# Kernel tuning notes

Hardware: AMD Instinct MI355X
Metric: run time of the kernel (lower is better)

The kernel has to match this reference:

```python
import jax, jax.numpy as jnp
import numpy as np

# ---- quantization scales (per-tensor, as produced by from_float calibration) ----
IN_SCALE = 0.05      # ForwardTokenizer: fp32 hidden -> int8
ALPHA_Q = 1e-4       # W8A8B8O8 requant multipliers (already include 1/sqrt(head_dim) for q)
ALPHA_K = 1e-4
ALPHA_V = 1e-4
QK_ALPHA = 1e-3      # BMM_S8T_S8N_F32T dequant scale (q_scale * k_scale)
PV_ALPHA = 1.0/127.0 # BMM_S8T_S8N_S8T requant scale ((1/127)*v_scale/out_scale)
OUT_ALPHA = 1e-4     # W8A8BFP32OFP32 dequant scale
NUM_HEADS = 32


def _quant_i8(x, scale):
    # simulate int8 quantization in fp32 (values are exact small integers)
    return jnp.clip(jnp.round(x / scale), -128.0, 127.0)


def _w8a8b8o8(x_i8, W_i8, b_i8, alpha):
    # int8 GEMM with int8 bias, requantized to int8: clamp(round(alpha*(x@W^T) + b))
    acc = jnp.einsum('btd,ed->bte', x_i8, W_i8)  # int32 accumulator in fp32
    return jnp.clip(jnp.round(alpha * acc + b_i8), -128.0, 127.0)


def setup_inputs() -> dict:
    key = jax.random.key(0)
    ks = jax.random.split(key, 10)
    B, T, D = 2, 2048, 2560
    hidden_states = jax.random.normal(ks[0], (B, T, D), dtype=jnp.float32)
    # causal additive mask, shape (B,1,T,T)
    neg = jnp.float32(-1e9)
    causal = jnp.where(jnp.tril(jnp.ones((T, T), dtype=bool)), 0.0, neg)
    attention_mask = jnp.broadcast_to(causal[None, None], (B, 1, T, T)).astype(jnp.float32)
    # int8-valued weights/biases stored as fp32 integers in [-127,127]
    def i8(k, shape):
        return jax.random.randint(k, shape, -127, 128).astype(jnp.float32)
    Wq = i8(ks[1], (D, D)); bq = i8(ks[2], (D,))
    Wk = i8(ks[3], (D, D)); bk = i8(ks[4], (D,))
    Wv = i8(ks[5], (D, D)); bv = i8(ks[6], (D,))
    Wo = i8(ks[7], (D, D))
    bo = jax.random.normal(ks[8], (D,), dtype=jnp.float32) * 0.01  # fp32 out bias
    return {"hidden_states": hidden_states, "attention_mask": attention_mask,
            "Wq": Wq, "bq": bq, "Wk": Wk, "bk": bk, "Wv": Wv, "bv": bv,
            "Wo": Wo, "bo": bo}


def reference(hidden_states, attention_mask, Wq, bq, Wk, bk, Wv, bv, Wo, bo):
    B, T, D = hidden_states.shape
    H = NUM_HEADS
    Dh = D // H
    # ForwardTokenizer: fp32 -> int8
    x_i8 = _quant_i8(hidden_states, IN_SCALE)
    # fused int8 q/k/v projections (W8A8B8O8Linear)
    q = _w8a8b8o8(x_i8, Wq, bq, ALPHA_Q)
    k = _w8a8b8o8(x_i8, Wk, bk, ALPHA_K)
    v = _w8a8b8o8(x_i8, Wv, bv, ALPHA_V)
    # (B,T,D) -> (B,H,T,Dh)
    def shape(t):
        return t.reshape(B, T, H, Dh).transpose(0, 2, 1, 3)
    q, k, v = shape(q), shape(k), shape(v)
    # BMM_S8T_S8N_F32T: int8 q @ k^T dequantized to fp32
    attn_weights = QK_ALPHA * jnp.einsum('bhqd,bhkd->bhqk', q, k)
    attn_weights = attn_weights + attention_mask  # (B,H,T,T)
    attn_weights = jnp.maximum(attn_weights, jnp.finfo(jnp.float32).min)
    attn_probs = jax.nn.softmax(attn_weights, axis=-1)
    # requantize probs to int8: mul_(127).round_()
    p_i8 = jnp.round(attn_probs * 127.0)
    # BMM_S8T_S8N_S8T: int8 p @ v requantized to int8
    attn_out = jnp.clip(jnp.round(PV_ALPHA * jnp.einsum('bhqk,bhkd->bhqd', p_i8, v)), -128.0, 127.0)
    # (B,H,T,Dh) -> (B,T,D)
    attn_out = attn_out.transpose(0, 2, 1, 3).reshape(B, T, D)
    # W8A8BFP32OFP32Linear: int8 GEMM, fp32 dequant + fp32 bias
    out = OUT_ALPHA * jnp.einsum('btd,ed->bte', attn_out, Wo) + bo
    return out
```

## Files before the change

kernel.cpp:

```cpp
#include <hip/hip_runtime.h>
#include <stdint.h>

typedef int v4i __attribute__((ext_vector_type(4)));

#define MFMA_I8(a,b,c) __builtin_amdgcn_mfma_i32_16x16x64_i8(a,b,c,0,0,0)

#define TD 2560
#define TT 2048
#define TB 2
#define TH 32
#define TDH 80
#define TDHP 128
#define TM 4096

#define LOG2E_MS 1.4426950408889634e-3f
#define MASKI (-(1<<30))

__device__ __forceinline__ float clamp8f(float v){ return fminf(fmaxf(v, -128.0f), 127.0f); }
__device__ __forceinline__ float fexp2(float x){ return __builtin_amdgcn_exp2f(x); }

__device__ __forceinline__ void gl_lds16(const int8_t* g, int8_t* l){
  __builtin_amdgcn_global_load_lds(
      (const __attribute__((address_space(1))) void*)g,
      (__attribute__((address_space(3))) void*)l, 16, 0, 0);
}

__global__ void k_quant(const float* __restrict__ x, int8_t* __restrict__ y, int n4){
  int stride = gridDim.x * blockDim.x;
  for (int i = blockIdx.x*blockDim.x + threadIdx.x; i < n4; i += stride){
    float4 v = ((const float4*)x)[i];
    char4 o;
    o.x = (int8_t)clamp8f(rintf(__fdiv_rn(v.x, 0.05f)));
    o.y = (int8_t)clamp8f(rintf(__fdiv_rn(v.y, 0.05f)));
    o.z = (int8_t)clamp8f(rintf(__fdiv_rn(v.z, 0.05f)));
    o.w = (int8_t)clamp8f(rintf(__fdiv_rn(v.w, 0.05f)));
    ((char4*)y)[i] = o;
  }
}

__global__ void k_conv(const float* __restrict__ w, int8_t* __restrict__ y, int n4){
  int stride = gridDim.x * blockDim.x;
  for (int i = blockIdx.x*blockDim.x + threadIdx.x; i < n4; i += stride){
    float4 v = ((const float4*)w)[i];
    char4 o;
    o.x = (int8_t)(int)rintf(v.x);
    o.y = (int8_t)(int)rintf(v.y);
    o.z = (int8_t)(int)rintf(v.z);
    o.w = (int8_t)(int)rintf(v.w);
    ((char4*)y)[i] = o;
  }
}

__global__ __launch_bounds__(256, 2) void k_gemm128(const int8_t* __restrict__ x,
    const int8_t* __restrict__ w, const float* __restrict__ bias,
    void* __restrict__ dst, int mode)
{
  __shared__ __align__(16) int8_t As[128*64];
  __shared__ __align__(16) int8_t Bs[128*64];
  const int m0 = blockIdx.x * 128, n0 = blockIdx.y * 128;
  const int t = threadIdx.x;
  const int wv = t >> 6, l = t & 63, lhi = (l >> 4) & 3, llo = l & 15;
  const int wr = wv >> 1, wc = wv & 1;
  const int grow = l >> 2, gcol = (l & 3) * 16;

  const int8_t* xa0 = x + (size_t)(m0 + wv*16 + grow)*TD + gcol;
  const int8_t* xa1 = x + (size_t)(m0 + 64 + wv*16 + grow)*TD + gcol;
  const int8_t* wb0 = w + (size_t)(n0 + wv*16 + grow)*TD + gcol;
  const int8_t* wb1 = w + (size_t)(n0 + 64 + wv*16 + grow)*TD + gcol;
  int8_t* la0 = &As[(wv*16)*64];
  int8_t* la1 = &As[(64 + wv*16)*64];
  int8_t* lb0 = &Bs[(wv*16)*64];
  int8_t* lb1 = &Bs[(64 + wv*16)*64];

  v4i acc[4][4] = {};
  for (int k0 = 0; k0 < TD; k0 += 64){
    gl_lds16(xa0 + k0, la0);
    gl_lds16(xa1 + k0, la1);
    gl_lds16(wb0 + k0, lb0);
    gl_lds16(wb1 + k0, lb1);
    __syncthreads();
    v4i a[4], b[4];
    #pragma unroll
    for (int mi = 0; mi < 4; ++mi)
      a[mi] = *(const v4i*)&As[(wr*64 + mi*16 + llo)*64 + lhi*16];
    #pragma unroll
    for (int ni = 0; ni < 4; ++ni)
      b[ni] = *(const v4i*)&Bs[(wc*64 + ni*16 + llo)*64 + lhi*16];
    #pragma unroll
    for (int mi = 0; mi < 4; ++mi)
      #pragma unroll
      for (int ni = 0; ni < 4; ++ni)
        acc[mi][ni] = MFMA_I8(a[mi], b[ni], acc[mi][ni]);
    __syncthreads();
  }

  #pragma unroll
  for (int mi = 0; mi < 4; ++mi)
  #pragma unroll
  for (int ni = 0; ni < 4; ++ni)
  #pragma unroll
  for (int r = 0; r < 4; ++r){
    int rowg = m0 + wr*64 + mi*16 + lhi*4 + r;
    int colg = n0 + wc*64 + ni*16 + llo;
    float fv = __fadd_rn(__fmul_rn(1e-4f, (float)acc[mi][ni][r]), bias[colg]);
    if (mode == 2){
      ((float*)dst)[(size_t)rowg*TD + colg] = fv;
    } else {
      int8_t q8 = (int8_t)clamp8f(rintf(fv));
      int bb = rowg >> 11, tl = rowg & 2047;
      int hh = colg / 80, dh = colg - hh*80;
      if (mode == 0) ((int8_t*)dst)[((size_t)(bb*TH + hh)*TT + tl)*TDHP + dh] = q8;
      else           ((int8_t*)dst)[((size_t)(bb*TH + hh)*TDH + dh)*TT + tl] = q8;
    }
  }
}

__global__ __launch_bounds__(256, 4) void k_attn5(const int8_t* __restrict__ qb_,
    const int8_t* __restrict__ kb_, const int8_t* __restrict__ vt_,
    int8_t* __restrict__ ao)
{
  __shared__ __align__(16) int8_t Ks[64*128];
  const int flat = blockIdx.x;
  const int g = flat & 7, ii = flat >> 3;
  const int pair = g*8 + (ii >> 4);
  const int j = ii & 15;
  const int h = pair & 31, b = pair >> 5;

  const int t = threadIdx.x, wv = t >> 6, l = t & 63, lhi = (l >> 4) & 3, llo = l & 15;
  const size_t bh = (size_t)(b*TH + h);
  const int8_t* qb = qb_ + bh*TT*TDHP;
  const int8_t* kb = kb_ + bh*TT*TDHP;
  const int8_t* vb = vt_ + bh*TDH*TT;

  const int srow = t >> 2, scp = (t & 3) * 2, ssw = srow & 7;
  const int8_t* kg = kb + (size_t)srow*TDHP + scp*16;
  int8_t* sdst0 = &Ks[srow*128 + (((scp  ) ^ ssw) << 4)];
  int8_t* sdst1 = &Ks[srow*128 + (((scp+1) ^ ssw) << 4)];

  #pragma unroll 1
  for (int half = 0; half < 2; ++half){
    const int qt2 = half ? j : (31 - j);
    const int qw0 = qt2*64 + wv*16;
    const int qg = qw0 + llo;
    const int ktmax = qt2 + 1;

    v4i qa0 = *(const v4i*)(qb + (size_t)(qw0 + llo)*TDHP + lhi*16);
    v4i qa1 = *(const v4i*)(qb + (size_t)(qw0 + llo)*TDHP + 64 + lhi*16);

    int   M  = MASKI;
    float cm = __fmul_rn(LOG2E_MS, (float)MASKI);
    float ls = 0.0f;

    v4i pr0 = *(const v4i*)(kg);
    v4i pr1 = *(const v4i*)(kg + 16);
    *(v4i*)sdst0 = pr0; *(v4i*)sdst1 = pr1;
    for (int kt = 0; kt < ktmax; ++kt){
      if (kt + 1 < ktmax){
        pr0 = *(const v4i*)(kg + (size_t)(kt+1)*64*TDHP);
        pr1 = *(const v4i*)(kg + (size_t)(kt+1)*64*TDHP + 16);
      }
      __syncthreads();
      const int rem = qw0 + 15 - kt*64;
      int sv[4][4];
      #pragma unroll
      for (int sub = 0; sub < 4; ++sub){
        if (sub*16 <= rem){
          const int row = sub*16 + llo, sw = row & 7;
          v4i kf0 = *(const v4i*)&Ks[row*128 + (((lhi  ) ^ sw) << 4)];
          v4i kf1 = *(const v4i*)&Ks[row*128 + (((lhi+4) ^ sw) << 4)];
          v4i d = {}; d = MFMA_I8(kf0, qa0, d); d = MFMA_I8(kf1, qa1, d);
          const int base = kt*64 + sub*16 + lhi*4;
          #pragma unroll
          for (int r = 0; r < 4; ++r)
            sv[sub][r] = (base + r <= qg) ? d[r] : MASKI;
        } else {
          #pragma unroll
          for (int r = 0; r < 4; ++r) sv[sub][r] = MASKI;
        }
      }
      int t0 = max(sv[0][0], sv[0][1]), t1 = max(sv[0][2], sv[0][3]);
      int t2 = max(sv[1][0], sv[1][1]), t3 = max(sv[1][2], sv[1][3]);
      int t4 = max(sv[2][0], sv[2][1]), t5 = max(sv[2][2], sv[2][3]);
      int t6 = max(sv[3][0], sv[3][1]), t7 = max(sv[3][2], sv[3][3]);
      int tm = max(max(max(t0,t1),max(t2,t3)), max(max(t4,t5),max(t6,t7)));
      int Mn = max(M, tm);
      float cmN = __fmul_rn(LOG2E_MS, (float)Mn);
      float fac = fexp2(__fsub_rn(cm, cmN));
      float e[16];
      #pragma unroll
      for (int sub = 0; sub < 4; ++sub)
        #pragma unroll
        for (int r = 0; r < 4; ++r)
          e[sub*4+r] = fexp2(__fmaf_rn((float)sv[sub][r], LOG2E_MS, -cmN));
      float a01 = __fadd_rn(e[0],e[1]),  a23 = __fadd_rn(e[2],e[3]);
      float a45 = __fadd_rn(e[4],e[5]),  a67 = __fadd_rn(e[6],e[7]);
      float a89 = __fadd_rn(e[8],e[9]),  aab = __fadd_rn(e[10],e[11]);
      float acd = __fadd_rn(e[12],e[13]), aef = __fadd_rn(e[14],e[15]);
      float b0 = __fadd_rn(a01,a23), b1 = __fadd_rn(a45,a67);
      float b2 = __fadd_rn(a89,aab), b3 = __fadd_rn(acd,aef);
      float tot = __fadd_rn(__fadd_rn(b0,b1), __fadd_rn(b2,b3));
      ls = __fadd_rn(__fmul_rn(ls, fac), tot);
      M = Mn; cm = cmN;
      __syncthreads();
      if (kt + 1 < ktmax){ *(v4i*)sdst0 = pr0; *(v4i*)sdst1 = pr1; }
    }

    {
      float mm = cm, ll = ls;
      #pragma unroll
      for (int off = 16; off < 64; off <<= 1){
        float om = __shfl_xor(mm, off);
        float ol = __shfl_xor(ll, off);
        float mn = fmaxf(mm, om);
        ll = __fadd_rn(__fmul_rn(ll, fexp2(__fsub_rn(mm, mn))),
                       __fmul_rn(ol, fexp2(__fsub_rn(om, mn))));
        mm = mn;
      }
      cm = mm;
      ls = __fdiv_rn(127.0f, ll);
    }

    v4i pacc[5] = {};
    pr0 = *(const v4i*)(kg);
    pr1 = *(const v4i*)(kg + 16);
    *(v4i*)sdst0 = pr0; *(v4i*)sdst1 = pr1;
    for (int kt = 0; kt < ktmax; ++kt){
      if (kt + 1 < ktmax){
        pr0 = *(const v4i*)(kg + (size_t)(kt+1)*64*TDHP);
        pr1 = *(const v4i*)(kg + (size_t)(kt+1)*64*TDHP + 16);
      }
      __syncthreads();
      const int rem = qw0 + 15 - kt*64;
      uint32_t w[4] = {0u,0u,0u,0u};
      #pragma unroll
      for (int sub = 0; sub < 4; ++sub){
        if (sub*16 <= rem){
          const int row = sub*16 + llo, sw = row & 7;
          v4i kf0 = *(const v4i*)&Ks[row*128 + (((lhi  ) ^ sw) << 4)];
          v4i kf1 = *(const v4i*)&Ks[row*128 + (((lhi+4) ^ sw) << 4)];
          v4i d = {}; d = MFMA_I8(kf0, qa0, d); d = MFMA_I8(kf1, qa1, d);
          const int base = kt*64 + sub*16 + lhi*4;
          uint32_t wrd = 0u;
          #pragma unroll
          for (int r = 0; r < 4; ++r){
            int sel = (base + r <= qg) ? d[r] : MASKI;
            float ev = fexp2(__fmaf_rn((float)sel, LOG2E_MS, -cm));
            int p = (int)rintf(__fmul_rn(ev, ls));
            wrd |= ((uint32_t)(uint8_t)p) << (8*r);
          }
          w[sub] = wrd;
        }
      }
      #pragma unroll
      for (int bb = 0; bb < 2; ++bb){
        const int dist = 16 << bb;
        const int gb = (lhi >> bb) & 1;
        uint32_t nw[4];
        #pragma unroll
        for (int s = 0; s < 4; ++s){
          uint32_t tv = __shfl_xor(w[s ^ (1 << bb)], dist);
          nw[s] = (((s >> bb) & 1) == gb) ? w[s] : tv;
        }
        w[0]=nw[0]; w[1]=nw[1]; w[2]=nw[2]; w[3]=nw[3];
      }
      v4i pa;
      pa[0]=(int)w[0]; pa[1]=(int)w[1]; pa[2]=(int)w[2]; pa[3]=(int)w[3];
      #pragma unroll
      for (int dt = 0; dt < 5; ++dt){
        v4i vf = *(const v4i*)(vb + (size_t)(dt*16 + llo)*TT + kt*64 + lhi*16);
        pacc[dt] = MFMA_I8(vf, pa, pacc[dt]);
      }
      __syncthreads();
      if (kt + 1 < ktmax){ *(v4i*)sdst0 = pr0; *(v4i*)sdst1 = pr1; }
    }

    #pragma unroll
    for (int dt = 0; dt < 5; ++dt){
      uint32_t ob = 0u;
      #pragma unroll
      for (int r = 0; r < 4; ++r){
        int vq = (int)clamp8f(rintf(__fmul_rn((float)pacc[dt][r], (float)(1.0/127.0))));
        ob |= ((uint32_t)(uint8_t)(int8_t)vq) << (8*r);
      }
      *(uint32_t*)(ao + ((size_t)(b*TT) + qw0 + llo)*TD + h*TDH + dt*16 + lhi*4) = ob;
    }
  }
}

extern "C" void kernel_launch(void* const* d_in, const int* in_sizes, int n_in,
                              void* d_out, int out_size, void* d_ws, size_t ws_size,
                              hipStream_t stream) {
  const float* hidden = (const float*)d_in[0];
  const float* Wq = (const float*)d_in[2];
  const float* bq = (const float*)d_in[3];
  const float* Wk = (const float*)d_in[4];
  const float* bk = (const float*)d_in[5];
  const float* Wv = (const float*)d_in[6];
  const float* bv = (const float*)d_in[7];
  const float* Wo = (const float*)d_in[8];
  const float* bo = (const float*)d_in[9];
  float* out = (float*)d_out;

  char* ws = (char*)d_ws;
  const size_t SZ_X  = (size_t)TM * TD;
  const size_t SZ_W  = (size_t)TD * TD;
  const size_t SZ_QK = (size_t)TB * TH * TT * TDHP;
  const size_t SZ_V  = (size_t)TB * TH * TDH * TT;
  int8_t* x8   = (int8_t*)ws;
  int8_t* wq8  = (int8_t*)(ws + SZ_X);
  int8_t* wk8  = wq8 + SZ_W;
  int8_t* wv8  = wk8 + SZ_W;
  int8_t* wo8  = wv8 + SZ_W;
  int8_t* qpad = wo8 + SZ_W;
  int8_t* kpad = qpad + SZ_QK;
  int8_t* vt   = kpad + SZ_QK;
  int8_t* ao   = vt + SZ_V;

  k_quant<<<4096, 256, 0, stream>>>(hidden, x8, (int)(SZ_X/4));
  k_conv<<<2048, 256, 0, stream>>>(Wq, wq8, (int)(SZ_W/4));
  k_conv<<<2048, 256, 0, stream>>>(Wk, wk8, (int)(SZ_W/4));
  k_conv<<<2048, 256, 0, stream>>>(Wv, wv8, (int)(SZ_W/4));
  k_conv<<<2048, 256, 0, stream>>>(Wo, wo8, (int)(SZ_W/4));
  hipMemsetAsync(qpad, 0, 2*SZ_QK, stream);

  k_gemm128<<<dim3(TM/128, TD/128), 256, 0, stream>>>(x8, wq8, bq, qpad, 0);
  k_gemm128<<<dim3(TM/128, TD/128), 256, 0, stream>>>(x8, wk8, bk, kpad, 0);
  k_gemm128<<<dim3(TM/128, TD/128), 256, 0, stream>>>(x8, wv8, bv, vt, 1);

  k_attn5<<<dim3(1024), 256, 0, stream>>>(qpad, kpad, vt, ao);

  k_gemm128<<<dim3(TM/128, TD/128), 256, 0, stream>>>(ao, wo8, bo, out, 2);
}
```

Measured before the change: 352.2 us.

## Merge projection launches, drop pad memset, split attention into per-tile blocks

The four weight conversions now run as one launch, and the Q/K/V GEMMs run as one 3D-grid launch. The output projection becomes its own specialised kernel. The memset of the padded Q/K buffers is removed: the upper half of each Q fragment is zeroed or loaded only for the lanes holding real head dimensions, so padding never affects results. The attention kernel moves from paired causal halves per block to one query tile per block, largest tiles first, with 2048 blocks and a higher occupancy bound. It also gains an unmasked fast path for full key tiles, precomputed swizzled LDS offsets, and magic-number float-to-int rounding for the probabilities. Each block now handles a single tile, so load balance depends on launch order rather than on pairing.

```diff
diff --git a/kernel.cpp b/kernel.cpp
--- a/kernel.cpp
+++ b/kernel.cpp
@@ -15,6 +15,7 @@
 
 #define LOG2E_MS 1.4426950408889634e-3f
 #define MASKI (-(1<<30))
+#define MAGICF 12582912.0f
 
 __device__ __forceinline__ float clamp8f(float v){ return fminf(fmaxf(v, -128.0f), 127.0f); }
 __device__ __forceinline__ float fexp2(float x){ return __builtin_amdgcn_exp2f(x); }
@@ -38,7 +39,13 @@
   }
 }
 
-__global__ void k_conv(const float* __restrict__ w, int8_t* __restrict__ y, int n4){
+__global__ void k_conv4(const float* __restrict__ w0, const float* __restrict__ w1,
+                        const float* __restrict__ w2, const float* __restrict__ w3,
+                        int8_t* __restrict__ y0, int8_t* __restrict__ y1,
+                        int8_t* __restrict__ y2, int8_t* __restrict__ y3, int n4){
+  const int z = blockIdx.y;
+  const float* w = z == 0 ? w0 : (z == 1 ? w1 : (z == 2 ? w2 : w3));
+  int8_t* y = z == 0 ? y0 : (z == 1 ? y1 : (z == 2 ? y2 : y3));
   int stride = gridDim.x * blockDim.x;
   for (int i = blockIdx.x*blockDim.x + threadIdx.x; i < n4; i += stride){
     float4 v = ((const float4*)w)[i];
@@ -51,9 +58,74 @@
   }
 }
 
-__global__ __launch_bounds__(256, 2) void k_gemm128(const int8_t* __restrict__ x,
-    const int8_t* __restrict__ w, const float* __restrict__ bias,
-    void* __restrict__ dst, int mode)
+__global__ __launch_bounds__(256, 2) void k_qkvg(const int8_t* __restrict__ x,
+    const int8_t* __restrict__ w0_, const int8_t* __restrict__ w1_, const int8_t* __restrict__ w2_,
+    const float* __restrict__ b0_, const float* __restrict__ b1_, const float* __restrict__ b2_,
+    int8_t* __restrict__ dq, int8_t* __restrict__ dk, int8_t* __restrict__ dv)
+{
+  __shared__ __align__(16) int8_t As[128*64];
+  __shared__ __align__(16) int8_t Bs[128*64];
+  const int z = blockIdx.z;
+  const int8_t* w = z == 0 ? w0_ : (z == 1 ? w1_ : w2_);
+  const float* bias = z == 0 ? b0_ : (z == 1 ? b1_ : b2_);
+  const int m0 = blockIdx.x * 128, n0 = blockIdx.y * 128;
+  const int t = threadIdx.x;
+  const int wv = t >> 6, l = t & 63, lhi = (l >> 4) & 3, llo = l & 15;
+  const int wr = wv >> 1, wc = wv & 1;
+  const int grow = l >> 2, gcol = (l & 3) * 16;
+
+  const int8_t* xa0 = x + (size_t)(m0 + wv*16 + grow)*TD + gcol;
+  const int8_t* xa1 = x + (size_t)(m0 + 64 + wv*16 + grow)*TD + gcol;
+  const int8_t* wb0 = w + (size_t)(n0 + wv*16 + grow)*TD + gcol;
+  const int8_t* wb1 = w + (size_t)(n0 + 64 + wv*16 + grow)*TD + gcol;
+  int8_t* la0 = &As[(wv*16)*64];
+  int8_t* la1 = &As[(64 + wv*16)*64];
+  int8_t* lb0 = &Bs[(wv*16)*64];
+  int8_t* lb1 = &Bs[(64 + wv*16)*64];
+
+  v4i acc[4][4] = {};
+  for (int k0 = 0; k0 < TD; k0 += 64){
+    gl_lds16(xa0 + k0, la0);
+    gl_lds16(xa1 + k0, la1);
+    gl_lds16(wb0 + k0, lb0);
+    gl_lds16(wb1 + k0, lb1);
+    __syncthreads();
+    v4i a[4], b[4];
+    #pragma unroll
+    for (int mi = 0; mi < 4; ++mi)
+      a[mi] = *(const v4i*)&As[(wr*64 + mi*16 + llo)*64 + lhi*16];
+    #pragma unroll
+    for (int ni = 0; ni < 4; ++ni)
+      b[ni] = *(const v4i*)&Bs[(wc*64 + ni*16 + llo)*64 + lhi*16];
+    #pragma unroll
+    for (int mi = 0; mi < 4; ++mi)
+      #pragma unroll
+      for (int ni = 0; ni < 4; ++ni)
+        acc[mi][ni] = MFMA_I8(a[mi], b[ni], acc[mi][ni]);
+    __syncthreads();
+  }
+
+  #pragma unroll
+  for (int mi = 0; mi < 4; ++mi)
+  #pragma unroll
+  for (int ni = 0; ni < 4; ++ni)
+  #pragma unroll
+  for (int r = 0; r < 4; ++r){
+    int rowg = m0 + wr*64 + mi*16 + lhi*4 + r;
+    int colg = n0 + wc*64 + ni*16 + llo;
+    float fv = __fadd_rn(__fmul_rn(1e-4f, (float)acc[mi][ni][r]), bias[colg]);
+    int8_t q8 = (int8_t)clamp8f(rintf(fv));
+    int bb = rowg >> 11, tl = rowg & 2047;
+    int hh = colg / 80, dh = colg - hh*80;
+    if (z == 0)      dq[((size_t)(bb*TH + hh)*TT + tl)*TDHP + dh] = q8;
+    else if (z == 1) dk[((size_t)(bb*TH + hh)*TT + tl)*TDHP + dh] = q8;
+    else             dv[((size_t)(bb*TH + hh)*TDH + dh)*TT + tl] = q8;
+  }
+}
+
+__global__ __launch_bounds__(256, 2) void k_oproj128(const int8_t* __restrict__ x,
+    const int8_t* __restrict__ w, const float* __restrict__ bo,
+    float* __restrict__ out)
 {
   __shared__ __align__(16) int8_t As[128*64];
   __shared__ __align__(16) int8_t Bs[128*64];
@@ -102,28 +174,20 @@
   for (int r = 0; r < 4; ++r){
     int rowg = m0 + wr*64 + mi*16 + lhi*4 + r;
     int colg = n0 + wc*64 + ni*16 + llo;
-    float fv = __fadd_rn(__fmul_rn(1e-4f, (float)acc[mi][ni][r]), bias[colg]);
-    if (mode == 2){
-      ((float*)dst)[(size_t)rowg*TD + colg] = fv;
-    } else {
-      int8_t q8 = (int8_t)clamp8f(rintf(fv));
-      int bb = rowg >> 11, tl = rowg & 2047;
-      int hh = colg / 80, dh = colg - hh*80;
-      if (mode == 0) ((int8_t*)dst)[((size_t)(bb*TH + hh)*TT + tl)*TDHP + dh] = q8;
-      else           ((int8_t*)dst)[((size_t)(bb*TH + hh)*TDH + dh)*TT + tl] = q8;
-    }
-  }
-}
-
-__global__ __launch_bounds__(256, 4) void k_attn5(const int8_t* __restrict__ qb_,
+    out[(size_t)rowg*TD + colg] =
+        __fadd_rn(__fmul_rn(1e-4f, (float)acc[mi][ni][r]), bo[colg]);
+  }
+}
+
+__global__ __launch_bounds__(256, 6) void k_attn6(const int8_t* __restrict__ qb_,
     const int8_t* __restrict__ kb_, const int8_t* __restrict__ vt_,
     int8_t* __restrict__ ao)
 {
   __shared__ __align__(16) int8_t Ks[64*128];
   const int flat = blockIdx.x;
   const int g = flat & 7, ii = flat >> 3;
-  const int pair = g*8 + (ii >> 4);
-  const int j = ii & 15;
+  const int qt = 31 - (ii >> 3);
+  const int pair = g*8 + (ii & 7);
   const int h = pair & 31, b = pair >> 5;
 
   const int t = threadIdx.x, wv = t >> 6, l = t & 63, lhi = (l >> 4) & 3, llo = l & 15;
@@ -132,42 +196,55 @@
   const int8_t* kb = kb_ + bh*TT*TDHP;
   const int8_t* vb = vt_ + bh*TDH*TT;
 
+  const int qw0 = qt*64 + wv*16;
+  const int qg = qw0 + llo;
+  const int ktmax = qt + 1;
+
+  int koff0[4], koff1[4];
+  #pragma unroll
+  for (int sub = 0; sub < 4; ++sub){
+    const int row = sub*16 + llo, sw = row & 7;
+    koff0[sub] = row*128 + (((lhi  ) ^ sw) << 4);
+    koff1[sub] = row*128 + (((lhi+4) ^ sw) << 4);
+  }
+
+  v4i qa0 = *(const v4i*)(qb + (size_t)(qw0 + llo)*TDHP + lhi*16);
+  v4i qa1 = {0,0,0,0};
+  if (lhi == 0) qa1 = *(const v4i*)(qb + (size_t)(qw0 + llo)*TDHP + 64);
+
   const int srow = t >> 2, scp = (t & 3) * 2, ssw = srow & 7;
   const int8_t* kg = kb + (size_t)srow*TDHP + scp*16;
   int8_t* sdst0 = &Ks[srow*128 + (((scp  ) ^ ssw) << 4)];
   int8_t* sdst1 = &Ks[srow*128 + (((scp+1) ^ ssw) << 4)];
 
-  #pragma unroll 1
-  for (int half = 0; half < 2; ++half){
-    const int qt2 = half ? j : (31 - j);
-    const int qw0 = qt2*64 + wv*16;
-    const int qg = qw0 + llo;
-    const int ktmax = qt2 + 1;
-
-    v4i qa0 = *(const v4i*)(qb + (size_t)(qw0 + llo)*TDHP + lhi*16);
-    v4i qa1 = *(const v4i*)(qb + (size_t)(qw0 + llo)*TDHP + 64 + lhi*16);
-
-    int   M  = MASKI;
-    float cm = __fmul_rn(LOG2E_MS, (float)MASKI);
-    float ls = 0.0f;
-
-    v4i pr0 = *(const v4i*)(kg);
-    v4i pr1 = *(const v4i*)(kg + 16);
-    *(v4i*)sdst0 = pr0; *(v4i*)sdst1 = pr1;
-    for (int kt = 0; kt < ktmax; ++kt){
-      if (kt + 1 < ktmax){
-        pr0 = *(const v4i*)(kg + (size_t)(kt+1)*64*TDHP);
-        pr1 = *(const v4i*)(kg + (size_t)(kt+1)*64*TDHP + 16);
+  int   M  = MASKI;
+  float cm = __fmul_rn(LOG2E_MS, (float)MASKI);
+  float ls = 0.0f;
+
+  v4i pr0 = *(const v4i*)(kg);
+  v4i pr1 = *(const v4i*)(kg + 16);
+  *(v4i*)sdst0 = pr0; *(v4i*)sdst1 = pr1;
+  for (int kt = 0; kt < ktmax; ++kt){
+    if (kt + 1 < ktmax){
+      pr0 = *(const v4i*)(kg + (size_t)(kt+1)*64*TDHP);
+      pr1 = *(const v4i*)(kg + (size_t)(kt+1)*64*TDHP + 16);
+    }
+    __syncthreads();
+    int sv[4][4];
+    if (kt < qt){
+      #pragma unroll
+      for (int sub = 0; sub < 4; ++sub){
+        v4i kf0 = *(const v4i*)&Ks[koff0[sub]];
+        v4i kf1 = *(const v4i*)&Ks[koff1[sub]];
+        v4i d = {}; d = MFMA_I8(kf0, qa0, d); d = MFMA_I8(kf1, qa1, d);
+        sv[sub][0]=d[0]; sv[sub][1]=d[1]; sv[sub][2]=d[2]; sv[sub][3]=d[3];
       }
-      __syncthreads();
-      const int rem = qw0 + 15 - kt*64;
-      int sv[4][4];
+    } else {
       #pragma unroll
       for (int sub = 0; sub < 4; ++sub){
-        if (sub*16 <= rem){
-          const int row = sub*16 + llo, sw = row & 7;
-          v4i kf0 = *(const v4i*)&Ks[row*128 + (((lhi  ) ^ sw) << 4)];
-          v4i kf1 = *(const v4i*)&Ks[row*128 + (((lhi+4) ^ sw) << 4)];
+        if (sub <= wv){
+          v4i kf0 = *(const v4i*)&Ks[koff0[sub]];
+          v4i kf1 = *(const v4i*)&Ks[koff1[sub]];
           v4i d = {}; d = MFMA_I8(kf0, qa0, d); d = MFMA_I8(kf1, qa1, d);
           const int base = kt*64 + sub*16 + lhi*4;
           #pragma unroll
@@ -178,112 +255,122 @@
           for (int r = 0; r < 4; ++r) sv[sub][r] = MASKI;
         }
       }
-      int t0 = max(sv[0][0], sv[0][1]), t1 = max(sv[0][2], sv[0][3]);
-      int t2 = max(sv[1][0], sv[1][1]), t3 = max(sv[1][2], sv[1][3]);
-      int t4 = max(sv[2][0], sv[2][1]), t5 = max(sv[2][2], sv[2][3]);
-      int t6 = max(sv[3][0], sv[3][1]), t7 = max(sv[3][2], sv[3][3]);
-      int tm = max(max(max(t0,t1),max(t2,t3)), max(max(t4,t5),max(t6,t7)));
-      int Mn = max(M, tm);
-      float cmN = __fmul_rn(LOG2E_MS, (float)Mn);
-      float fac = fexp2(__fsub_rn(cm, cmN));
-      float e[16];
-      #pragma unroll
-      for (int sub = 0; sub < 4; ++sub)
-        #pragma unroll
-        for (int r = 0; r < 4; ++r)
-          e[sub*4+r] = fexp2(__fmaf_rn((float)sv[sub][r], LOG2E_MS, -cmN));
-      float a01 = __fadd_rn(e[0],e[1]),  a23 = __fadd_rn(e[2],e[3]);
-      float a45 = __fadd_rn(e[4],e[5]),  a67 = __fadd_rn(e[6],e[7]);
-      float a89 = __fadd_rn(e[8],e[9]),  aab = __fadd_rn(e[10],e[11]);
-      float acd = __fadd_rn(e[12],e[13]), aef = __fadd_rn(e[14],e[15]);
-      float b0 = __fadd_rn(a01,a23), b1 = __fadd_rn(a45,a67);
-      float b2 = __fadd_rn(a89,aab), b3 = __fadd_rn(acd,aef);
-      float tot = __fadd_rn(__fadd_rn(b0,b1), __fadd_rn(b2,b3));
-      ls = __fadd_rn(__fmul_rn(ls, fac), tot);
-      M = Mn; cm = cmN;
-      __syncthreads();
-      if (kt + 1 < ktmax){ *(v4i*)sdst0 = pr0; *(v4i*)sdst1 = pr1; }
-    }
-
-    {
-      float mm = cm, ll = ls;
-      #pragma unroll
-      for (int off = 16; off < 64; off <<= 1){
-        float om = __shfl_xor(mm, off);
-        float ol = __shfl_xor(ll, off);
-        float mn = fmaxf(mm, om);
-        ll = __fadd_rn(__fmul_rn(ll, fexp2(__fsub_rn(mm, mn))),
-                       __fmul_rn(ol, fexp2(__fsub_rn(om, mn))));
-        mm = mn;
+    }
+    int m0 = max(max(sv[0][0], sv[0][1]), sv[0][2]);
+    int m1 = max(max(sv[0][3], sv[1][0]), sv[1][1]);
+    int m2 = max(max(sv[1][2], sv[1][3]), sv[2][0]);
+    int m3 = max(max(sv[2][1], sv[2][2]), sv[2][3]);
+    int m4 = max(max(sv[3][0], sv[3][1]), sv[3][2]);
+    int tm = max(max(max(m0, m1), max(m2, m3)), max(m4, sv[3][3]));
+    int Mn = max(M, tm);
+    float cmN = __fmul_rn(LOG2E_MS, (float)Mn);
+    float fac = fexp2(__fsub_rn(cm, cmN));
+    float tot = 0.0f;
+    #pragma unroll
+    for (int sub = 0; sub < 4; ++sub){
+      float e0 = fexp2(__fmaf_rn((float)sv[sub][0], LOG2E_MS, -cmN));
+      float e1 = fexp2(__fmaf_rn((float)sv[sub][1], LOG2E_MS, -cmN));
+      float e2 = fexp2(__fmaf_rn((float)sv[sub][2], LOG2E_MS, -cmN));
+      float e3 = fexp2(__fmaf_rn((float)sv[sub][3], LOG2E_MS, -cmN));
+      tot = __fadd_rn(tot, __fadd_rn(__fadd_rn(e0, e1), __fadd_rn(e2, e3)));
+    }
+    ls = __fmaf_rn(ls, fac, tot);
+    M = Mn; cm = cmN;
+    __syncthreads();
+    if (kt + 1 < ktmax){ *(v4i*)sdst0 = pr0; *(v4i*)sdst1 = pr1; }
+  }
+
+  float rq;
+  {
+    float mm = cm, ll = ls;
+    #pragma unroll
+    for (int off = 16; off < 64; off <<= 1){
+      float om = __shfl_xor(mm, off);
+      float ol = __shfl_xor(ll, off);
+      float mn = fmaxf(mm, om);
+      ll = __fadd_rn(__fmul_rn(ll, fexp2(__fsub_rn(mm, mn))),
+                     __fmul_rn(ol, fexp2(__fsub_rn(om, mn))));
+      mm = mn;
+    }
+    cm = mm;
+    rq = __fdiv_rn(127.0f, ll);
+  }
+
+  v4i pacc[5] = {};
+  pr0 = *(const v4i*)(kg);
+  pr1 = *(const v4i*)(kg + 16);
+  __syncthreads();
+  *(v4i*)sdst0 = pr0; *(v4i*)sdst1 = pr1;
+  for (int kt = 0; kt < ktmax; ++kt){
+    if (kt + 1 < ktmax){
+      pr0 = *(const v4i*)(kg + (size_t)(kt+1)*64*TDHP);
+      pr1 = *(const v4i*)(kg + (size_t)(kt+1)*64*TDHP + 16);
+    }
+    __syncthreads();
+    uint32_t w[4] = {0u,0u,0u,0u};
+    if (kt < qt){
+      #pragma unroll
+      for (int sub = 0; sub < 4; ++sub){
+        v4i kf0 = *(const v4i*)&Ks[koff0[sub]];
+        v4i kf1 = *(const v4i*)&Ks[koff1[sub]];
+        v4i d = {}; d = MFMA_I8(kf0, qa0, d); d = MFMA_I8(kf1, qa1, d);
+        uint32_t u0 = __float_as_uint(__fmaf_rn(fexp2(__fmaf_rn((float)d[0], LOG2E_MS, -cm)), rq, MAGICF));
+        uint32_t u1 = __float_as_uint(__fmaf_rn(fexp2(__fmaf_rn((float)d[1], LOG2E_MS, -cm)), rq, MAGICF));
+        uint32_t u2 = __float_as_uint(__fmaf_rn(fexp2(__fmaf_rn((float)d[2], LOG2E_MS, -cm)), rq, MAGICF));
+        uint32_t u3 = __float_as_uint(__fmaf_rn(fexp2(__fmaf_rn((float)d[3], LOG2E_MS, -cm)), rq, MAGICF));
+        w[sub] = (u0 & 0xffu) | ((u1 & 0xffu) << 8) | ((u2 & 0xffu) << 16) | (u3 << 24);
       }
-      cm = mm;
-      ls = __fdiv_rn(127.0f, ll);
-    }
-
-    v4i pacc[5] = {};
-    pr0 = *(const v4i*)(kg);
-    pr1 = *(const v4i*)(kg + 16);
-    *(v4i*)sdst0 = pr0; *(v4i*)sdst1 = pr1;
-    for (int kt = 0; kt < ktmax; ++kt){
-      if (kt + 1 < ktmax){
-        pr0 = *(const v4i*)(kg + (size_t)(kt+1)*64*TDHP);
-        pr1 = *(const v4i*)(kg + (size_t)(kt+1)*64*TDHP + 16);
-      }
-      __syncthreads();
-      const int rem = qw0 + 15 - kt*64;
-      uint32_t w[4] = {0u,0u,0u,0u};
+    } else {
       #pragma unroll
       for (int sub = 0; sub < 4; ++sub){
-        if (sub*16 <= rem){
-          const int row = sub*16 + llo, sw = row & 7;
-          v4i kf0 = *(const v4i*)&Ks[row*128 + (((lhi  ) ^ sw) << 4)];
-          v4i kf1 = *(const v4i*)&Ks[row*128 + (((lhi+4) ^ sw) << 4)];
+        if (sub <= wv){
+          v4i kf0 = *(const v4i*)&Ks[koff0[sub]];
+          v4i kf1 = *(const v4i*)&Ks[koff1[sub]];
           v4i d = {}; d = MFMA_I8(kf0, qa0, d); d = MFMA_I8(kf1, qa1, d);
           const int base = kt*64 + sub*16 + lhi*4;
           uint32_t wrd = 0u;
           #pragma unroll
           for (int r = 0; r < 4; ++r){
             int sel = (base + r <= qg) ? d[r] : MASKI;
-            float ev = fexp2(__fmaf_rn((float)sel, LOG2E_MS, -cm));
-            int p = (int)rintf(__fmul_rn(ev, ls));
-            wrd |= ((uint32_t)(uint8_t)p) << (8*r);
+            uint32_t u = __float_as_uint(__fmaf_rn(fexp2(__fmaf_rn((float)sel, LOG2E_MS, -cm)), rq, MAGICF));
+            wrd |= (u & 0xffu) << (8*r);
           }
           w[sub] = wrd;
         }
       }
-      #pragma unroll
-      for (int bb = 0; bb < 2; ++bb){
-        const int dist = 16 << bb;
-        const int gb = (lhi >> bb) & 1;
-        uint32_t nw[4];
-        #pragma unroll
-        for (int s = 0; s < 4; ++s){
-          uint32_t tv = __shfl_xor(w[s ^ (1 << bb)], dist);
-          nw[s] = (((s >> bb) & 1) == gb) ? w[s] : tv;
-        }
-        w[0]=nw[0]; w[1]=nw[1]; w[2]=nw[2]; w[3]=nw[3];
+    }
+    #pragma unroll
+    for (int bb = 0; bb < 2; ++bb){
+      const int dist = 16 << bb;
+      const int gb = (lhi >> bb) & 1;
+      uint32_t nw[4];
+      #pragma unroll
+      for (int s = 0; s < 4; ++s){
+        uint32_t tv = __shfl_xor(w[s ^ (1 << bb)], dist);
+        nw[s] = (((s >> bb) & 1) == gb) ? w[s] : tv;
       }
-      v4i pa;
-      pa[0]=(int)w[0]; pa[1]=(int)w[1]; pa[2]=(int)w[2]; pa[3]=(int)w[3];
-      #pragma unroll
-      for (int dt = 0; dt < 5; ++dt){
-        v4i vf = *(const v4i*)(vb + (size_t)(dt*16 + llo)*TT + kt*64 + lhi*16);
-        pacc[dt] = MFMA_I8(vf, pa, pacc[dt]);
-      }
-      __syncthreads();
-      if (kt + 1 < ktmax){ *(v4i*)sdst0 = pr0; *(v4i*)sdst1 = pr1; }
-    }
-
+      w[0]=nw[0]; w[1]=nw[1]; w[2]=nw[2]; w[3]=nw[3];
+    }
+    v4i pa;
+    pa[0]=(int)w[0]; pa[1]=(int)w[1]; pa[2]=(int)w[2]; pa[3]=(int)w[3];
     #pragma unroll
     for (int dt = 0; dt < 5; ++dt){
-      uint32_t ob = 0u;
-      #pragma unroll
-      for (int r = 0; r < 4; ++r){
-        int vq = (int)clamp8f(rintf(__fmul_rn((float)pacc[dt][r], (float)(1.0/127.0))));
-        ob |= ((uint32_t)(uint8_t)(int8_t)vq) << (8*r);
-      }
-      *(uint32_t*)(ao + ((size_t)(b*TT) + qw0 + llo)*TD + h*TDH + dt*16 + lhi*4) = ob;
-    }
+      v4i vf = *(const v4i*)(vb + (size_t)(dt*16 + llo)*TT + kt*64 + lhi*16);
+      pacc[dt] = MFMA_I8(vf, pa, pacc[dt]);
+    }
+    __syncthreads();
+    if (kt + 1 < ktmax){ *(v4i*)sdst0 = pr0; *(v4i*)sdst1 = pr1; }
+  }
+
+  #pragma unroll
+  for (int dt = 0; dt < 5; ++dt){
+    uint32_t ob = 0u;
+    #pragma unroll
+    for (int r = 0; r < 4; ++r){
+      int vq = (int)clamp8f(rintf(__fmul_rn((float)pacc[dt][r], (float)(1.0/127.0))));
+      ob |= ((uint32_t)(uint8_t)(int8_t)vq) << (8*r);
+    }
+    *(uint32_t*)(ao + ((size_t)(b*TT) + qw0 + llo)*TD + h*TDH + dt*16 + lhi*4) = ob;
   }
 }
 
@@ -317,17 +404,12 @@
   int8_t* ao   = vt + SZ_V;
 
   k_quant<<<4096, 256, 0, stream>>>(hidden, x8, (int)(SZ_X/4));
-  k_conv<<<2048, 256, 0, stream>>>(Wq, wq8, (int)(SZ_W/4));
-  k_conv<<<2048, 256, 0, stream>>>(Wk, wk8, (int)(SZ_W/4));
-  k_conv<<<2048, 256, 0, stream>>>(Wv, wv8, (int)(SZ_W/4));
-  k_conv<<<2048, 256, 0, stream>>>(Wo, wo8, (int)(SZ_W/4));
-  hipMemsetAsync(qpad, 0, 2*SZ_QK, stream);
-
-  k_gemm128<<<dim3(TM/128, TD/128), 256, 0, stream>>>(x8, wq8, bq, qpad, 0);
-  k_gemm128<<<dim3(TM/128, TD/128), 256, 0, stream>>>(x8, wk8, bk, kpad, 0);
-  k_gemm128<<<dim3(TM/128, TD/128), 256, 0, stream>>>(x8, wv8, bv, vt, 1);
-
-  k_attn5<<<dim3(1024), 256, 0, stream>>>(qpad, kpad, vt, ao);
-
-  k_gemm128<<<dim3(TM/128, TD/128), 256, 0, stream>>>(ao, wo8, bo, out, 2);
-}
+  k_conv4<<<dim3(1024, 4), 256, 0, stream>>>(Wq, Wk, Wv, Wo, wq8, wk8, wv8, wo8, (int)(SZ_W/4));
+
+  k_qkvg<<<dim3(TM/128, TD/128, 3), 256, 0, stream>>>(x8, wq8, wk8, wv8, bq, bk, bv,
+                                                      qpad, kpad, vt);
+
+  k_attn6<<<dim3(2048), 256, 0, stream>>>(qpad, kpad, vt, ao);
+
+  k_oproj128<<<dim3(TM/128, TD/128), 256, 0, stream>>>(ao, wo8, bo, out);
+}
```

Result: faster. 312.5 us (-11.3%).
